# Optimization experiments

Hardware: AMD Instinct MI355X
Metric: run time of the kernel (lower is better)

The kernel has to match this reference:

```python
import jax, jax.numpy as jnp
import numpy as np

TOP_K = 2


def setup_inputs() -> dict:
    key = jax.random.key(0)
    ks = jax.random.split(key, 5)
    B, S, D, F, E = 2, 2048, 1024, 3584, 8
    scale_in = 1.0 / np.sqrt(D)
    scale_f = 1.0 / np.sqrt(F)
    return {
        "hidden_states": jax.random.normal(ks[0], (B, S, D), dtype=jnp.float32),
        "gate_w": jax.random.normal(ks[1], (E, D), dtype=jnp.float32) * scale_in,
        "w1": jax.random.normal(ks[2], (E, F, D), dtype=jnp.float32) * scale_in,
        "w3": jax.random.normal(ks[3], (E, F, D), dtype=jnp.float32) * scale_in,
        "w2": jax.random.normal(ks[4], (E, D, F), dtype=jnp.float32) * scale_f,
    }


def _routing_weights(logits):
    # softmax over experts, select top-k, renormalize (Mixtral semantics)
    probs = jax.nn.softmax(logits, axis=-1)          # [T, E]
    topv, topi = jax.lax.top_k(probs, TOP_K)          # [T, k]
    topv = topv / jnp.sum(topv, axis=-1, keepdims=True)
    T, E = logits.shape
    w = jnp.zeros((T, E), dtype=logits.dtype)
    w = w.at[jnp.arange(T)[:, None], topi].set(topv)  # dense [T, E] routing weights
    return w


def reference(hidden_states, gate_w, w1, w3, w2):
    B, S, D = hidden_states.shape
    x = hidden_states.reshape(-1, D)                  # [T, D]
    logits = x @ gate_w.T                             # [T, E]
    rw = _routing_weights(logits)                     # [T, E]
    E = gate_w.shape[0]
    out = jnp.zeros_like(x)
    for e in range(E):                                # fixed small expert count
        h = jax.nn.silu(x @ w1[e].T) * (x @ w3[e].T)  # [T, F]
        out = out + rw[:, e:e + 1] * (h @ w2[e].T)    # [T, D]
    return out.reshape(B, S, D)
```

## Files before the change

kernel.cpp:

```cpp
#include <hip/hip_runtime.h>
#include <hip/hip_bf16.h>


#define T_TOK 4096
#define DIM   1024
#define FF    3584
#define NE    8
#define CAP   (T_TOK*2 + NE*256)

#define OFF_TOPI   256UL
#define OFF_TOPW   33024UL
#define OFF_ROWTOK 65792UL
#define OFF_ROWW   106752UL
#define OFF_W13    147712UL
#define OFF_W2B    OFF_W13
#define OFF_H      (OFF_W13 + 117440512UL)
#define WS_NEED    (OFF_H + 73400320UL)

using f32x4 = __attribute__((ext_vector_type(4))) float;
using s16x8 = __attribute__((ext_vector_type(8))) short;

__device__ __forceinline__ ushort f2b(float f) {
    __hip_bfloat16 b = __float2bfloat16(f);
    ushort u; __builtin_memcpy(&u, &b, 2); return u;
}
__device__ __forceinline__ void gl_lds16(const ushort* g, ushort* l) {
    __builtin_amdgcn_global_load_lds(
        (const __attribute__((address_space(1))) void*)g,
        (__attribute__((address_space(3))) void*)l, 16, 0, 0);
}
__device__ __forceinline__ uint4 pack8(float4 v0, float4 v1) {
    uint4 o;
    o.x = f2b(v0.x) | ((uint)f2b(v0.y) << 16);
    o.y = f2b(v0.z) | ((uint)f2b(v0.w) << 16);
    o.z = f2b(v1.x) | ((uint)f2b(v1.y) << 16);
    o.w = f2b(v1.z) | ((uint)f2b(v1.w) << 16);
    return o;
}

#define LGKM0 do { asm volatile("s_waitcnt lgkmcnt(0)" ::: "memory"); \
                   __builtin_amdgcn_sched_barrier(0); } while (0)
#define VMC(n) asm volatile("s_waitcnt vmcnt(" #n ")" ::: "memory")
#define BAR()  __builtin_amdgcn_s_barrier()

__global__ __launch_bounds__(256)
void k_route(const float* __restrict__ x, const float* __restrict__ gw,
             int* __restrict__ topi, float* __restrict__ topw, int* __restrict__ counts)
{
    __shared__ float gws[NE*DIM];
    const int tid = threadIdx.x;
    for (int i = tid; i < NE*DIM/4; i += 256)
        ((float4*)gws)[i] = ((const float4*)gw)[i];
    __syncthreads();

    const int lane = tid & 63, wid = tid >> 6;
    const int t = blockIdx.x*4 + wid;

    float4 xr[4];
    const float4* xrow = (const float4*)(x + (size_t)t*DIM) + lane*4;
    #pragma unroll
    for (int i = 0; i < 4; ++i) xr[i] = xrow[i];

    float lg[NE];
    #pragma unroll
    for (int e = 0; e < NE; ++e) {
        const float4* g4 = (const float4*)(gws + e*DIM) + lane*4;
        float s = 0.f;
        #pragma unroll
        for (int i = 0; i < 4; ++i) {
            float4 g = g4[i];
            s += xr[i].x*g.x + xr[i].y*g.y + xr[i].z*g.z + xr[i].w*g.w;
        }
        #pragma unroll
        for (int off = 32; off; off >>= 1) s += __shfl_xor(s, off);
        lg[e] = s;
    }
    if (lane == 0) {
        float b1 = -1e30f, b2 = -1e30f; int i1 = 0, i2 = 0;
        #pragma unroll
        for (int e = 0; e < NE; ++e) {
            float v = lg[e];
            if (v > b1)      { b2 = b1; i2 = i1; b1 = v; i1 = e; }
            else if (v > b2) { b2 = v; i2 = e; }
        }
        float p2 = __expf(b2 - b1);
        float inv = 1.f / (1.f + p2);
        topi[2*t]   = i1; topi[2*t+1] = i2;
        topw[2*t]   = inv; topw[2*t+1] = p2*inv;
        atomicAdd(&counts[i1], 1); atomicAdd(&counts[i2], 1);
    }
}

__global__ void k_scan(const int* __restrict__ counts, int* __restrict__ offs,
                       int* __restrict__ rowTok)
{
    if (threadIdx.x == 0) {
        int acc = 0; offs[0] = 0;
        for (int e = 0; e < NE; ++e) {
            int p = (counts[e] + 255) & ~255;
            acc += p; offs[e+1] = acc;
        }
    }
    for (int i = threadIdx.x; i < CAP; i += blockDim.x) rowTok[i] = -1;
}

__global__ __launch_bounds__(256)
void k_scatter(const int* __restrict__ topi, const float* __restrict__ topw,
               const int* __restrict__ offs, int* __restrict__ cursor,
               int* __restrict__ rowTok, float* __restrict__ rowW)
{
    int t = blockIdx.x*256 + threadIdx.x;
    #pragma unroll
    for (int j = 0; j < 2; ++j) {
        int e = topi[2*t + j];
        int pos = offs[e] + atomicAdd(&cursor[e], 1);
        rowTok[pos] = t;
        rowW[pos] = topw[2*t + j];
    }
}

__global__ __launch_bounds__(256)
void k_cvt(const float* __restrict__ src, ushort* __restrict__ dst)
{
    size_t i = (size_t)blockIdx.x*256 + threadIdx.x;
    float4 v0 = ((const float4*)src)[2*i], v1 = ((const float4*)src)[2*i+1];
    ((uint4*)dst)[i] = pack8(v0, v1);
}

__global__ __launch_bounds__(256)
void k_cvt13(const float* __restrict__ w1, const float* __restrict__ w3,
             ushort* __restrict__ w13)
{
    int i = blockIdx.x*256 + threadIdx.x;
    int k8 = i & 127;
    int r  = i >> 7;
    int rd = r & 127;
    int sb = (r >> 7) % 56;
    int e  = r / 7168;
    int f  = sb*64 + (rd >> 5)*16 + (rd & 15);
    const float* src = (((rd >> 4) & 1) ? w3 : w1) + ((size_t)e*FF + f)*DIM + k8*8;
    float4 v0 = ((const float4*)src)[0], v1 = ((const float4*)src)[1];
    ((uint4*)w13)[i] = pack8(v0, v1);
}

#define G1_SLOT 12288
__global__ __launch_bounds__(256, 2)
void k_gemm1(const ushort* __restrict__ xb, const ushort* __restrict__ w13,
             const int* __restrict__ offs, const int* __restrict__ rowTok,
             ushort* __restrict__ hout)
{
    __shared__ __align__(16) ushort L[3*G1_SLOT];
    const int rowStart = blockIdx.y * 256;
    if (rowStart >= offs[8]) return;
    int e = 0;
    #pragma unroll
    for (int k = 1; k < NE; ++k) if (rowStart >= offs[k]) e = k;
    const int sb = blockIdx.x;
    const ushort* __restrict__ Wb = w13 + (((size_t)e*56 + sb) * 128) * DIM;

    const int tid = threadIdx.x, lane = tid & 63, wid = tid >> 6;
    const int wr = wid >> 1, wc = wid & 1;
    const int lo = lane & 15, hi = lane >> 4;

    const int srow = lane >> 2;
    const int sch  = (lane & 3) ^ ((lane >> 3) & 3);
    const ushort* aS[4];
    #pragma unroll
    for (int j = 0; j < 4; ++j) {
        int tk = rowTok[rowStart + j*64 + wid*16 + srow]; if (tk < 0) tk = 0;
        aS[j] = xb + (size_t)tk*DIM + sch*8;
    }
    const ushort* bS[2];
    #pragma unroll
    for (int j = 0; j < 2; ++j)
        bS[j] = Wb + (size_t)(j*64 + wid*16 + srow)*DIM + sch*8;
    ushort* const dA = L + wid*512;
    ushort* const dB = L + 8192 + wid*512;

    const int sig = (lo >> 1) & 3;
    const int roff = ((hi ^ sig) * 8);
    int rdA[8], rdB[4];
    #pragma unroll
    for (int m = 0; m < 8; ++m) rdA[m] = (wr*128 + m*16 + lo)*32 + roff;
    #pragma unroll
    for (int n = 0; n < 4; ++n) rdB[n] = 8192 + (wc*64 + n*16 + lo)*32 + roff;

    f32x4 acc[8][4];
    #pragma unroll
    for (int m = 0; m < 8; ++m)
        #pragma unroll
        for (int n = 0; n < 4; ++n) acc[m][n] = (f32x4)(0.f);

    #pragma unroll
    for (int t0 = 0; t0 < 2; ++t0) {
        #pragma unroll
        for (int j = 0; j < 4; ++j) gl_lds16(aS[j] + t0*32, dA + t0*G1_SLOT + j*2048);
        #pragma unroll
        for (int j = 0; j < 2; ++j) gl_lds16(bS[j] + t0*32, dB + t0*G1_SLOT + j*2048);
    }
    VMC(6);
    BAR();

    const int NK = DIM/32;
    int cur = 0, nxt = 2;
    for (int t = 0; t < NK; ++t) {
        const ushort* Lb = L + cur*G1_SLOT;
        const bool pf = (t + 2 < NK);
        s16x8 a[4], b[4];
        #pragma unroll
        for (int n = 0; n < 4; ++n) b[n] = *(const s16x8*)(Lb + rdB[n]);
        #pragma unroll
        for (int m = 0; m < 4; ++m) a[m] = *(const s16x8*)(Lb + rdA[m]);
        if (pf) {
            #pragma unroll
            for (int j = 0; j < 3; ++j)
                gl_lds16(aS[j] + (t+2)*32, dA + nxt*G1_SLOT + j*2048);
        }
        BAR();
        LGKM0;
        __builtin_amdgcn_s_setprio(1);
        #pragma unroll
        for (int m = 0; m < 4; ++m)
            #pragma unroll
            for (int n = 0; n < 4; ++n)
                acc[m][n] = __builtin_amdgcn_mfma_f32_16x16x32_bf16(a[m], b[n], acc[m][n], 0, 0, 0);
        __builtin_amdgcn_s_setprio(0);
        BAR();
        #pragma unroll
        for (int m = 0; m < 4; ++m) a[m] = *(const s16x8*)(Lb + rdA[4+m]);
        if (pf) {
            gl_lds16(aS[3] + (t+2)*32, dA + nxt*G1_SLOT + 3*2048);
            gl_lds16(bS[0] + (t+2)*32, dB + nxt*G1_SLOT);
            gl_lds16(bS[1] + (t+2)*32, dB + nxt*G1_SLOT + 2048);
        }
        BAR();
        LGKM0;
        __builtin_amdgcn_s_setprio(1);
        #pragma unroll
        for (int m = 0; m < 4; ++m)
            #pragma unroll
            for (int n = 0; n < 4; ++n)
                acc[4+m][n] = __builtin_amdgcn_mfma_f32_16x16x32_bf16(a[m], b[n], acc[4+m][n], 0, 0, 0);
        __builtin_amdgcn_s_setprio(0);
        if (t < NK-2) { VMC(6); } else { VMC(0); }
        BAR();
        cur = (cur == 2) ? 0 : cur + 1;
        nxt = (nxt == 2) ? 0 : nxt + 1;
    }

    #pragma unroll
    for (int m = 0; m < 8; ++m)
        #pragma unroll
        for (int p = 0; p < 2; ++p) {
            f32x4 v1 = acc[m][2*p], v3 = acc[m][2*p+1];
            int f = sb*64 + (wc*2 + p)*16 + lo;
            #pragma unroll
            for (int j = 0; j < 4; ++j) {
                int row = rowStart + wr*128 + m*16 + hi*4 + j;
                float s = v1[j];
                float val = (s / (1.f + __expf(-s))) * v3[j];
                hout[(size_t)row*FF + f] = f2b(val);
            }
        }
}

#define G2_SLOT 8192
__global__ __launch_bounds__(256, 3)
void k_gemm2(const ushort* __restrict__ h, const ushort* __restrict__ w2b,
             const int* __restrict__ offs, const int* __restrict__ rowTok,
             const float* __restrict__ rowW, float* __restrict__ out)
{
    __shared__ __align__(16) ushort L[3*G2_SLOT];
    const int rowStart = blockIdx.y * 128;
    if (rowStart >= offs[8]) return;
    int e = 0;
    #pragma unroll
    for (int k = 1; k < NE; ++k) if (rowStart >= offs[k]) e = k;
    const int dc = blockIdx.x * 128;
    const ushort* __restrict__ W2 = w2b + ((size_t)e*DIM + dc)*FF;

    const int tid = threadIdx.x, lane = tid & 63, wid = tid >> 6;
    const int wr = wid >> 1, wc = wid & 1;
    const int lo = lane & 15, hi = lane >> 4;

    const int srow = lane >> 2;
    const int sch  = (lane & 3) ^ ((lane >> 3) & 3);
    const ushort* aS[2];
    const ushort* bS[2];
    #pragma unroll
    for (int j = 0; j < 2; ++j) {
        int r = j*64 + wid*16 + srow;
        aS[j] = h  + (size_t)(rowStart + r)*FF + sch*8;
        bS[j] = W2 + (size_t)r*FF + sch*8;
    }
    ushort* const dA = L + wid*512;
    ushort* const dB = L + 4096 + wid*512;

    const int sig = (lo >> 1) & 3;
    const int roff = ((hi ^ sig) * 8);
    int rdA[4], rdB[4];
    #pragma unroll
    for (int m = 0; m < 4; ++m) rdA[m] = (wr*64 + m*16 + lo)*32 + roff;
    #pragma unroll
    for (int n = 0; n < 4; ++n) rdB[n] = 4096 + (wc*64 + n*16 + lo)*32 + roff;

    f32x4 acc[4][4];
    #pragma unroll
    for (int m = 0; m < 4; ++m)
        #pragma unroll
        for (int n = 0; n < 4; ++n) acc[m][n] = (f32x4)(0.f);

    #pragma unroll
    for (int t0 = 0; t0 < 2; ++t0) {
        #pragma unroll
        for (int j = 0; j < 2; ++j) gl_lds16(aS[j] + t0*32, dA + t0*G2_SLOT + j*2048);
        #pragma unroll
        for (int j = 0; j < 2; ++j) gl_lds16(bS[j] + t0*32, dB + t0*G2_SLOT + j*2048);
    }
    VMC(4);
    BAR();

    const int NK = FF/32;
    int cur = 0, nxt = 2;
    for (int t = 0; t < NK; ++t) {
        const ushort* Lb = L + cur*G2_SLOT;
        const bool pf = (t + 2 < NK);
        s16x8 a[4], b[4];
        #pragma unroll
        for (int n = 0; n < 4; ++n) b[n] = *(const s16x8*)(Lb + rdB[n]);
        #pragma unroll
        for (int m = 0; m < 4; ++m) a[m] = *(const s16x8*)(Lb + rdA[m]);
        if (pf) {
            #pragma unroll
            for (int j = 0; j < 2; ++j) gl_lds16(aS[j] + (t+2)*32, dA + nxt*G2_SLOT + j*2048);
            #pragma unroll
            for (int j = 0; j < 2; ++j) gl_lds16(bS[j] + (t+2)*32, dB + nxt*G2_SLOT + j*2048);
        }
        BAR();
        LGKM0;
        __builtin_amdgcn_s_setprio(1);
        #pragma unroll
        for (int m = 0; m < 4; ++m)
            #pragma unroll
            for (int n = 0; n < 4; ++n)
                acc[m][n] = __builtin_amdgcn_mfma_f32_16x16x32_bf16(a[m], b[n], acc[m][n], 0, 0, 0);
        __builtin_amdgcn_s_setprio(0);
        if (t < NK-2) { VMC(4); } else { VMC(0); }
        BAR();
        cur = (cur == 2) ? 0 : cur + 1;
        nxt = (nxt == 2) ? 0 : nxt + 1;
    }

    #pragma unroll
    for (int m = 0; m < 4; ++m)
        #pragma unroll
        for (int j = 0; j < 4; ++j) {
            int prow = rowStart + wr*64 + m*16 + hi*4 + j;
            int tok = rowTok[prow];
            if (tok < 0) continue;
            float w = rowW[prow];
            #pragma unroll
            for (int n = 0; n < 4; ++n) {
                int d = dc + wc*64 + n*16 + lo;
                atomicAdd(&out[(size_t)tok*DIM + d], w * acc[m][n][j]);
            }
        }
}

extern "C" void kernel_launch(void* const* d_in, const int* in_sizes, int n_in,
                              void* d_out, int out_size, void* d_ws, size_t ws_size,
                              hipStream_t stream)
{
    const float* x  = (const float*)d_in[0];
    const float* gw = (const float*)d_in[1];
    const float* w1 = (const float*)d_in[2];
    const float* w3 = (const float*)d_in[3];
    const float* w2 = (const float*)d_in[4];
    float* out = (float*)d_out;
    char* ws = (char*)d_ws;
    if (ws_size < WS_NEED) return;

    int*    counts = (int*)ws;
    int*    cursor = counts + 8;
    int*    offs   = counts + 16;
    int*    topi   = (int*)  (ws + OFF_TOPI);
    float*  topw   = (float*)(ws + OFF_TOPW);
    int*    rowTok = (int*)  (ws + OFF_ROWTOK);
    float*  rowW   = (float*)(ws + OFF_ROWW);
    ushort* w13b   = (ushort*)(ws + OFF_W13);
    ushort* w2b    = (ushort*)(ws + OFF_W2B);
    ushort* h      = (ushort*)(ws + OFF_H);
    ushort* xb     = (ushort*)d_out;

    hipMemsetAsync(ws, 0, 256, stream);

    k_route  <<<T_TOK/4, 256, 0, stream>>>(x, gw, topi, topw, counts);
    k_scan   <<<1, 256, 0, stream>>>(counts, offs, rowTok);
    k_scatter<<<T_TOK/256, 256, 0, stream>>>(topi, topw, offs, cursor, rowTok, rowW);
    k_cvt    <<<(T_TOK*DIM/8)/256, 256, 0, stream>>>(x, xb);
    k_cvt13  <<<(2*NE*FF*DIM/8)/256, 256, 0, stream>>>(w1, w3, w13b);
    k_gemm1  <<<dim3(56, CAP/256), 256, 0, stream>>>(xb, w13b, offs, rowTok, h);
    k_cvt    <<<(NE*DIM*FF/8)/256, 256, 0, stream>>>(w2, w2b);
    hipMemsetAsync(d_out, 0, (size_t)T_TOK*DIM*4, stream);
    k_gemm2  <<<dim3(DIM/128, CAP/128), 256, 0, stream>>>(h, w2b, offs, rowTok, rowW, out);
}
```

Before: 514.3 us.

## Fuse x bf16 conversion into routing, split w1/w3 layouts, retile gemm2 to 2 waves

The router kernel now writes the bf16 copy of x itself, so the separate conversion pass is dropped. The interleaved w1/w3 repack kernel is replaced by two plain contiguous conversions, and gemm1 reads w1 and w3 rows from separate buffers. gemm2 is retiled to 128-thread blocks where each wave computes 64x128 with more accumulators, trading occupancy for register-level reuse of B fragments. Per-wave VGPR pressure in gemm2 rises and strided B loads in gemm1 may differ in locality.

```diff
diff --git a/kernel.cpp b/kernel.cpp
--- a/kernel.cpp
+++ b/kernel.cpp
@@ -12,9 +12,10 @@
 #define OFF_TOPW   33024UL
 #define OFF_ROWTOK 65792UL
 #define OFF_ROWW   106752UL
-#define OFF_W13    147712UL
-#define OFF_W2B    OFF_W13
-#define OFF_H      (OFF_W13 + 117440512UL)
+#define OFF_W1B    147712UL
+#define OFF_W3B    (OFF_W1B + 58720256UL)
+#define OFF_W2B    OFF_W1B
+#define OFF_H      (OFF_W1B + 117440512UL)
 #define WS_NEED    (OFF_H + 73400320UL)
 
 using f32x4 = __attribute__((ext_vector_type(4))) float;
@@ -45,7 +46,8 @@
 
 __global__ __launch_bounds__(256)
 void k_route(const float* __restrict__ x, const float* __restrict__ gw,
-             int* __restrict__ topi, float* __restrict__ topw, int* __restrict__ counts)
+             int* __restrict__ topi, float* __restrict__ topw,
+             int* __restrict__ counts, ushort* __restrict__ xb)
 {
     __shared__ float gws[NE*DIM];
     const int tid = threadIdx.x;
@@ -61,6 +63,10 @@
     #pragma unroll
     for (int i = 0; i < 4; ++i) xr[i] = xrow[i];
 
+    uint4* xbd = (uint4*)(xb + (size_t)t*DIM);
+    xbd[lane*2]   = pack8(xr[0], xr[1]);
+    xbd[lane*2+1] = pack8(xr[2], xr[3]);
+
     float lg[NE];
     #pragma unroll
     for (int e = 0; e < NE; ++e) {
@@ -127,36 +133,20 @@
     ((uint4*)dst)[i] = pack8(v0, v1);
 }
 
-__global__ __launch_bounds__(256)
-void k_cvt13(const float* __restrict__ w1, const float* __restrict__ w3,
-             ushort* __restrict__ w13)
-{
-    int i = blockIdx.x*256 + threadIdx.x;
-    int k8 = i & 127;
-    int r  = i >> 7;
-    int rd = r & 127;
-    int sb = (r >> 7) % 56;
-    int e  = r / 7168;
-    int f  = sb*64 + (rd >> 5)*16 + (rd & 15);
-    const float* src = (((rd >> 4) & 1) ? w3 : w1) + ((size_t)e*FF + f)*DIM + k8*8;
-    float4 v0 = ((const float4*)src)[0], v1 = ((const float4*)src)[1];
-    ((uint4*)w13)[i] = pack8(v0, v1);
-}
-
 #define G1_SLOT 12288
 __global__ __launch_bounds__(256, 2)
-void k_gemm1(const ushort* __restrict__ xb, const ushort* __restrict__ w13,
+void k_gemm1(const ushort* __restrict__ xb,
+             const ushort* __restrict__ w1b, const ushort* __restrict__ w3b,
              const int* __restrict__ offs, const int* __restrict__ rowTok,
              ushort* __restrict__ hout)
 {
     __shared__ __align__(16) ushort L[3*G1_SLOT];
+    const int sb = blockIdx.x;
     const int rowStart = blockIdx.y * 256;
     if (rowStart >= offs[8]) return;
     int e = 0;
     #pragma unroll
     for (int k = 1; k < NE; ++k) if (rowStart >= offs[k]) e = k;
-    const int sb = blockIdx.x;
-    const ushort* __restrict__ Wb = w13 + (((size_t)e*56 + sb) * 128) * DIM;
 
     const int tid = threadIdx.x, lane = tid & 63, wid = tid >> 6;
     const int wr = wid >> 1, wc = wid & 1;
@@ -171,9 +161,8 @@
         aS[j] = xb + (size_t)tk*DIM + sch*8;
     }
     const ushort* bS[2];
-    #pragma unroll
-    for (int j = 0; j < 2; ++j)
-        bS[j] = Wb + (size_t)(j*64 + wid*16 + srow)*DIM + sch*8;
+    bS[0] = w1b + ((size_t)e*FF + sb*64 + wid*16 + srow)*DIM + sch*8;
+    bS[1] = w3b + ((size_t)e*FF + sb*64 + wid*16 + srow)*DIM + sch*8;
     ushort* const dA = L + wid*512;
     ushort* const dB = L + 8192 + wid*512;
 
@@ -183,7 +172,10 @@
     #pragma unroll
     for (int m = 0; m < 8; ++m) rdA[m] = (wr*128 + m*16 + lo)*32 + roff;
     #pragma unroll
-    for (int n = 0; n < 4; ++n) rdB[n] = 8192 + (wc*64 + n*16 + lo)*32 + roff;
+    for (int n = 0; n < 2; ++n) {
+        rdB[n]   = 8192 + (wc*32 + n*16 + lo)*32 + roff;
+        rdB[n+2] = 8192 + (64 + wc*32 + n*16 + lo)*32 + roff;
+    }
 
     f32x4 acc[8][4];
     #pragma unroll
@@ -252,8 +244,8 @@
     for (int m = 0; m < 8; ++m)
         #pragma unroll
         for (int p = 0; p < 2; ++p) {
-            f32x4 v1 = acc[m][2*p], v3 = acc[m][2*p+1];
-            int f = sb*64 + (wc*2 + p)*16 + lo;
+            f32x4 v1 = acc[m][p], v3 = acc[m][p+2];
+            int f = sb*64 + wc*32 + p*16 + lo;
             #pragma unroll
             for (int j = 0; j < 4; ++j) {
                 int row = rowStart + wr*128 + m*16 + hi*4 + j;
@@ -264,77 +256,73 @@
         }
 }
 
-#define G2_SLOT 8192
-__global__ __launch_bounds__(256, 3)
+#define G2S 8192
+__global__ __launch_bounds__(128)
 void k_gemm2(const ushort* __restrict__ h, const ushort* __restrict__ w2b,
              const int* __restrict__ offs, const int* __restrict__ rowTok,
              const float* __restrict__ rowW, float* __restrict__ out)
 {
-    __shared__ __align__(16) ushort L[3*G2_SLOT];
+    __shared__ __align__(16) ushort L[3*G2S];
+    const int dc = blockIdx.x * 128;
     const int rowStart = blockIdx.y * 128;
     if (rowStart >= offs[8]) return;
     int e = 0;
     #pragma unroll
     for (int k = 1; k < NE; ++k) if (rowStart >= offs[k]) e = k;
-    const int dc = blockIdx.x * 128;
-    const ushort* __restrict__ W2 = w2b + ((size_t)e*DIM + dc)*FF;
-
-    const int tid = threadIdx.x, lane = tid & 63, wid = tid >> 6;
-    const int wr = wid >> 1, wc = wid & 1;
+
+    const int tid = threadIdx.x, lane = tid & 63, w = tid >> 6;
     const int lo = lane & 15, hi = lane >> 4;
 
     const int srow = lane >> 2;
     const int sch  = (lane & 3) ^ ((lane >> 3) & 3);
-    const ushort* aS[2];
-    const ushort* bS[2];
-    #pragma unroll
-    for (int j = 0; j < 2; ++j) {
-        int r = j*64 + wid*16 + srow;
-        aS[j] = h  + (size_t)(rowStart + r)*FF + sch*8;
-        bS[j] = W2 + (size_t)r*FF + sch*8;
-    }
-    ushort* const dA = L + wid*512;
-    ushort* const dB = L + 4096 + wid*512;
+    const ushort* aS[4]; const ushort* bS[4];
+    #pragma unroll
+    for (int j = 0; j < 4; ++j) {
+        int r = j*32 + w*16 + srow;
+        aS[j] = h   + (size_t)(rowStart + r)*FF + sch*8;
+        bS[j] = w2b + ((size_t)e*DIM + dc + r)*FF + sch*8;
+    }
 
     const int sig = (lo >> 1) & 3;
     const int roff = ((hi ^ sig) * 8);
-    int rdA[4], rdB[4];
-    #pragma unroll
-    for (int m = 0; m < 4; ++m) rdA[m] = (wr*64 + m*16 + lo)*32 + roff;
-    #pragma unroll
-    for (int n = 0; n < 4; ++n) rdB[n] = 4096 + (wc*64 + n*16 + lo)*32 + roff;
-
-    f32x4 acc[4][4];
+    int rdA[4], rdB[8];
+    #pragma unroll
+    for (int m = 0; m < 4; ++m) rdA[m] = (w*64 + m*16 + lo)*32 + roff;
+    #pragma unroll
+    for (int n = 0; n < 8; ++n) rdB[n] = 4096 + (n*16 + lo)*32 + roff;
+
+    f32x4 acc[4][8];
     #pragma unroll
     for (int m = 0; m < 4; ++m)
         #pragma unroll
-        for (int n = 0; n < 4; ++n) acc[m][n] = (f32x4)(0.f);
+        for (int n = 0; n < 8; ++n) acc[m][n] = (f32x4)(0.f);
 
     #pragma unroll
     for (int t0 = 0; t0 < 2; ++t0) {
         #pragma unroll
-        for (int j = 0; j < 2; ++j) gl_lds16(aS[j] + t0*32, dA + t0*G2_SLOT + j*2048);
-        #pragma unroll
-        for (int j = 0; j < 2; ++j) gl_lds16(bS[j] + t0*32, dB + t0*G2_SLOT + j*2048);
-    }
-    VMC(4);
+        for (int j = 0; j < 4; ++j) gl_lds16(aS[j] + t0*32, L + t0*G2S + j*1024 + w*512);
+        #pragma unroll
+        for (int j = 0; j < 4; ++j) gl_lds16(bS[j] + t0*32, L + t0*G2S + 4096 + j*1024 + w*512);
+    }
+    VMC(8);
     BAR();
 
     const int NK = FF/32;
     int cur = 0, nxt = 2;
     for (int t = 0; t < NK; ++t) {
-        const ushort* Lb = L + cur*G2_SLOT;
+        const ushort* Lb = L + cur*G2S;
+        ushort* Ln = L + nxt*G2S;
         const bool pf = (t + 2 < NK);
-        s16x8 a[4], b[4];
-        #pragma unroll
-        for (int n = 0; n < 4; ++n) b[n] = *(const s16x8*)(Lb + rdB[n]);
+        s16x8 a[4], b[8];
+        #pragma unroll
+        for (int n = 0; n < 8; ++n) b[n] = *(const s16x8*)(Lb + rdB[n]);
         #pragma unroll
         for (int m = 0; m < 4; ++m) a[m] = *(const s16x8*)(Lb + rdA[m]);
         if (pf) {
             #pragma unroll
-            for (int j = 0; j < 2; ++j) gl_lds16(aS[j] + (t+2)*32, dA + nxt*G2_SLOT + j*2048);
-            #pragma unroll
-            for (int j = 0; j < 2; ++j) gl_lds16(bS[j] + (t+2)*32, dB + nxt*G2_SLOT + j*2048);
+            for (int j = 0; j < 4; ++j) gl_lds16(aS[j] + (t+2)*32, Ln + j*1024 + w*512);
+            #pragma unroll
+            for (int j = 0; j < 4; ++j) gl_lds16(bS[j] + (t+2)*32, Ln + 4096 + j*1024 + w*512);
         }
         BAR();
         LGKM0;
@@ -342,10 +330,10 @@
         #pragma unroll
         for (int m = 0; m < 4; ++m)
             #pragma unroll
-            for (int n = 0; n < 4; ++n)
+            for (int n = 0; n < 8; ++n)
                 acc[m][n] = __builtin_amdgcn_mfma_f32_16x16x32_bf16(a[m], b[n], acc[m][n], 0, 0, 0);
         __builtin_amdgcn_s_setprio(0);
-        if (t < NK-2) { VMC(4); } else { VMC(0); }
+        if (t < NK-2) { VMC(8); } else { VMC(0); }
         BAR();
         cur = (cur == 2) ? 0 : cur + 1;
         nxt = (nxt == 2) ? 0 : nxt + 1;
@@ -355,14 +343,14 @@
     for (int m = 0; m < 4; ++m)
         #pragma unroll
         for (int j = 0; j < 4; ++j) {
-            int prow = rowStart + wr*64 + m*16 + hi*4 + j;
+            int prow = rowStart + w*64 + m*16 + hi*4 + j;
             int tok = rowTok[prow];
             if (tok < 0) continue;
-            float w = rowW[prow];
-            #pragma unroll
-            for (int n = 0; n < 4; ++n) {
-                int d = dc + wc*64 + n*16 + lo;
-                atomicAdd(&out[(size_t)tok*DIM + d], w * acc[m][n][j]);
+            float wgt = rowW[prow];
+            #pragma unroll
+            for (int n = 0; n < 8; ++n) {
+                int d = dc + n*16 + lo;
+                atomicAdd(&out[(size_t)tok*DIM + d], wgt * acc[m][n][j]);
             }
         }
 }
@@ -387,20 +375,21 @@
     float*  topw   = (float*)(ws + OFF_TOPW);
     int*    rowTok = (int*)  (ws + OFF_ROWTOK);
     float*  rowW   = (float*)(ws + OFF_ROWW);
-    ushort* w13b   = (ushort*)(ws + OFF_W13);
+    ushort* w1b    = (ushort*)(ws + OFF_W1B);
+    ushort* w3b    = (ushort*)(ws + OFF_W3B);
     ushort* w2b    = (ushort*)(ws + OFF_W2B);
     ushort* h      = (ushort*)(ws + OFF_H);
     ushort* xb     = (ushort*)d_out;
 
     hipMemsetAsync(ws, 0, 256, stream);
 
-    k_route  <<<T_TOK/4, 256, 0, stream>>>(x, gw, topi, topw, counts);
+    k_route  <<<T_TOK/4, 256, 0, stream>>>(x, gw, topi, topw, counts, xb);
     k_scan   <<<1, 256, 0, stream>>>(counts, offs, rowTok);
     k_scatter<<<T_TOK/256, 256, 0, stream>>>(topi, topw, offs, cursor, rowTok, rowW);
-    k_cvt    <<<(T_TOK*DIM/8)/256, 256, 0, stream>>>(x, xb);
-    k_cvt13  <<<(2*NE*FF*DIM/8)/256, 256, 0, stream>>>(w1, w3, w13b);
-    k_gemm1  <<<dim3(56, CAP/256), 256, 0, stream>>>(xb, w13b, offs, rowTok, h);
+    k_cvt    <<<(NE*FF*DIM/8)/256, 256, 0, stream>>>(w1, w1b);
+    k_cvt    <<<(NE*FF*DIM/8)/256, 256, 0, stream>>>(w3, w3b);
+    k_gemm1  <<<dim3(56, CAP/256), 256, 0, stream>>>(xb, w1b, w3b, offs, rowTok, h);
     k_cvt    <<<(NE*DIM*FF/8)/256, 256, 0, stream>>>(w2, w2b);
     hipMemsetAsync(d_out, 0, (size_t)T_TOK*DIM*4, stream);
-    k_gemm2  <<<dim3(DIM/128, CAP/128), 256, 0, stream>>>(h, w2b, offs, rowTok, rowW, out);
-}
+    k_gemm2  <<<dim3(DIM/128, CAP/128), 128, 0, stream>>>(h, w2b, offs, rowTok, rowW, out);
+}
```

New measurement: 539.3 us. 4.8% more time.
